# Kernel optimization log

Measured on AMD Instinct MI355X. Metric: run time of the kernel, lower is better.

The kernel has to match this reference:

```python
import jax, jax.numpy as jnp
import numpy as np

DIM, HEAD, R = 192, 8, 3
RR = 2 * R + 1
RA = RR * RR  # 49-sample local window


def conv2d(x, w, b):
    y = jax.lax.conv_general_dilated(x, w, (1, 1), 'SAME',
                                     dimension_numbers=('NCHW', 'OIHW', 'NCHW'))
    return y + b[None, :, None, None]


def _pix(c, size):
    # normalized [-1,1] -> pixel coord, align_corners=False
    return (c + 1.0) * (size * 0.5) - 0.5


def _gather(img, iy, ix, valid=None):
    # img [B,C,H,W]; iy/ix int [B,...] -> [B,C,...]; zero-fill where not valid
    B, C, H, W = img.shape
    sh = iy.shape
    idx = (jnp.clip(iy, 0, H - 1) * W + jnp.clip(ix, 0, W - 1)).reshape(B, -1)
    g = jax.vmap(lambda f, i: f[:, i])(img.reshape(B, C, H * W), idx)
    g = g.reshape((B, C) + sh[1:])
    if valid is not None:
        g = g * valid.reshape((B, 1) + sh[1:]).astype(g.dtype)
    return g


def bilinear_sample(img, cy, cx, border=False):
    # F.grid_sample bilinear, align_corners=False; cy/cx [B,Q] -> [B,C,Q]
    B, C, H, W = img.shape
    py, px = _pix(cy, H), _pix(cx, W)
    y0f, x0f = jnp.floor(py), jnp.floor(px)
    wy, wx = py - y0f, px - x0f
    y0, x0 = y0f.astype(jnp.int32), x0f.astype(jnp.int32)
    out = 0.0
    for dy, sy in ((0, 1.0 - wy), (1, wy)):
        for dx, sx in ((0, 1.0 - wx), (1, wx)):
            iy, ix = y0 + dy, x0 + dx
            valid = None if border else ((iy >= 0) & (iy < H) & (ix >= 0) & (ix < W))
            out = out + _gather(img, iy, ix, valid) * (sy * sx)[:, None]
    return out


def nearest_sample(img, cy, cx):
    # F.grid_sample nearest, align_corners=False, padding_mode='zeros'
    B, C, H, W = img.shape
    iy = jnp.floor(_pix(cy, H) + 0.5).astype(jnp.int32)
    ix = jnp.floor(_pix(cx, W) + 0.5).astype(jnp.int32)
    valid = (iy >= 0) & (iy < H) & (ix >= 0) & (ix < W)
    return _gather(img, iy, ix, valid)


def mlp(x, ws, bs):
    for w, b in zip(ws[:-1], bs[:-1]):
        x = jax.nn.relu(x @ w + b)
    return x @ ws[-1] + bs[-1]


def reference(inp, sample_coord, cell, enc_w, enc_b, ch_w, ch_b, q_w, q_b,
              k_w, k_b, v_w, v_b, m0w, m0b, m1w, m1b, m2w, m2b, m3w, m3b, m4w, m4b):
    # gen_feat: encoder (conv stand-in) -> conv_ch -> q/k/v convs
    feat = conv2d(conv2d(inp, enc_w, enc_b), ch_w, ch_b)
    feat_q = conv2d(feat, q_w, q_b)
    feat_k = conv2d(feat, k_w, k_b)
    feat_v = conv2d(feat, v_w, v_b)
    B, _, H, W = feat.shape
    Q = sample_coord.shape[1]
    hd = DIM // HEAD

    cy, cx = sample_coord[..., 0], sample_coord[..., 1]
    # sample_coord_k: nearest LR pixel-center coords (grid_sample nearest over make_coord grid)
    iy = jnp.clip(jnp.floor(_pix(cy, H) + 0.5), 0, H - 1)
    ix = jnp.clip(jnp.floor(_pix(cx, W) + 0.5), 0, W - 1)
    sky = -1.0 + (2.0 * iy + 1.0) / H
    skx = -1.0 + (2.0 * ix + 1.0) / W

    dh = jnp.linspace(-R, R, RR, dtype=jnp.float32) * (2.0 / H)
    dw = jnp.linspace(-R, R, RR, dtype=jnp.float32) * (2.0 / W)
    gy, gx = jnp.meshgrid(dh, dw, indexing='ij')
    cky = sky[..., None] + gy.reshape(-1)  # [B,Q,RA]
    ckx = skx[..., None] + gx.reshape(-1)

    q = bilinear_sample(feat_q, cy, cx)                       # [B,DIM,Q]
    q = q.transpose(0, 2, 1).reshape(B, Q, HEAD, hd)
    k = nearest_sample(feat_k, cky, ckx)                      # [B,DIM,Q,RA]
    k = k.transpose(0, 2, 3, 1).reshape(B, Q, RA, HEAD, hd)
    v = nearest_sample(feat_v, cky, ckx)
    v = v.transpose(0, 2, 3, 1).reshape(B, Q, RA, HEAD, hd)

    attn = jnp.einsum('bqhd,bqrhd->bqrh', q, k) / np.sqrt(hd).astype(np.float32)
    attn = jax.nn.softmax(attn, axis=2)                       # softmax over window
    v = (v * attn[..., None]).reshape(B, Q, RA * DIM)         # weighted, NOT summed

    rel_cell = cell[:, None, :] * jnp.array([H, W], jnp.float32)
    rel_cell = jnp.broadcast_to(rel_cell, (B, Q, 2))
    feat_in = jnp.concatenate([v, rel_cell], axis=-1)         # [B,Q,DIM*RA+2]

    pred = mlp(feat_in, [m0w, m1w, m2w, m3w, m4w], [m0b, m1b, m2b, m3b, m4b])
    base = bilinear_sample(inp, cy, cx, border=True).transpose(0, 2, 1)  # [B,Q,3]
    return pred + base


def setup_inputs() -> dict:
    key = jax.random.key(0)
    ks = jax.random.split(key, 16)
    B, H, W, Q = 2, 64, 64, 4096
    enc_out, hidden = 64, 256
    in_dim = DIM * RA + 2

    def cw(k, o, i):
        return jax.random.normal(k, (o, i, 3, 3), jnp.float32) / np.sqrt(i * 9.0)

    def lw(k, i, o):
        return jax.random.normal(k, (i, o), jnp.float32) / np.sqrt(float(i))

    return {
        'inp': jax.random.normal(ks[0], (B, 3, H, W), jnp.float32),
        'sample_coord': jax.random.uniform(ks[1], (B, Q, 2), jnp.float32, -1.0, 1.0),
        'cell': jnp.full((B, 2), 2.0 / 128.0, jnp.float32),
        'enc_w': cw(ks[2], enc_out, 3), 'enc_b': jnp.zeros((enc_out,), jnp.float32),
        'ch_w': cw(ks[3], DIM, enc_out), 'ch_b': jnp.zeros((DIM,), jnp.float32),
        'q_w': cw(ks[4], DIM, DIM), 'q_b': jnp.zeros((DIM,), jnp.float32),
        'k_w': cw(ks[5], DIM, DIM), 'k_b': jnp.zeros((DIM,), jnp.float32),
        'v_w': cw(ks[6], DIM, DIM), 'v_b': jnp.zeros((DIM,), jnp.float32),
        'm0w': lw(ks[7], in_dim, hidden), 'm0b': jnp.zeros((hidden,), jnp.float32),
        'm1w': lw(ks[8], hidden, hidden), 'm1b': jnp.zeros((hidden,), jnp.float32),
        'm2w': lw(ks[9], hidden, hidden), 'm2b': jnp.zeros((hidden,), jnp.float32),
        'm3w': lw(ks[10], hidden, hidden), 'm3b': jnp.zeros((hidden,), jnp.float32),
        'm4w': lw(ks[11], hidden, 3), 'm4b': jnp.zeros((3,), jnp.float32),
    }
```

## Files before the change

kernel.cpp:

```cpp
#include <hip/hip_runtime.h>
#include <hip/hip_bf16.h>


constexpr int BB = 2, QQ = 4096, DIMC = 192, RAW = 49;
constexpr int ENC = 64, P1 = 66, P3 = 70;

typedef __attribute__((ext_vector_type(8))) short bf16x8;
typedef __attribute__((ext_vector_type(8))) unsigned short u16x8;
typedef __attribute__((ext_vector_type(4))) float f32x4;

__device__ inline short f2bf(float f) {
  __hip_bfloat16 h = __float2bfloat16(f);
  return __builtin_bit_cast(short, h);
}
__device__ inline float bf2f(unsigned short u) {
  return __uint_as_float(((unsigned)u) << 16);
}

constexpr long long N_F1 = (long long)BB * P1 * P1 * ENC;
constexpr long long N_FT = (long long)BB * P1 * P1 * DIMC;
constexpr long long N_FKS = (long long)BB * P3 * P3 * DIMC;
constexpr long long F_F1 = 0;
constexpr long long F_FEAT = F_F1 + N_F1;
constexpr long long F_FQ = F_FEAT + N_FT;
constexpr long long F_FKB = F_FQ + N_FT;
constexpr long long F_FVB = F_FKB + N_FKS / 2;
constexpr long long F_ZEND = F_FVB + N_FKS / 2;
constexpr long long F_ATTN = F_ZEND;
constexpr long long F_HA = F_ATTN + (long long)BB * QQ * RAW * 8;
constexpr long long F_HB = F_HA + 8192LL * 256;
constexpr long long F_W0T = F_HB + 8192LL * 256;
constexpr long long F_WTCHB = F_W0T + (256LL * 9408) / 2;
constexpr long long F_WTQB = F_WTCHB + (192LL * 576) / 2;
constexpr long long F_WTKB = F_WTQB + (192LL * 1728) / 2;
constexpr long long F_WTVB = F_WTKB + (192LL * 1728) / 2;
constexpr long long ZERO_N4 = F_ZEND / 4;

__global__ __launch_bounds__(256) void k_zero(float4* p, int n4) {
  int i = blockIdx.x * 256 + threadIdx.x;
  float4 z = make_float4(0.f, 0.f, 0.f, 0.f);
  for (; i < n4; i += gridDim.x * 256) p[i] = z;
}

__global__ __launch_bounds__(256) void k_w0t(const float* __restrict__ w0,
                                             short* __restrict__ w0t) {
  __shared__ short sh[64][72];
  int k0 = blockIdx.x * 64, n0 = blockIdx.y * 64;
  int t = threadIdx.x;
  #pragma unroll
  for (int i = 0; i < 16; i++) {
    int idx = t + i * 256;
    int r = idx >> 6, cc = idx & 63;
    sh[cc][r] = f2bf(w0[(long long)(k0 + r) * 256 + n0 + cc]);
  }
  __syncthreads();
  #pragma unroll
  for (int i = 0; i < 16; i++) {
    int idx = t + i * 256;
    int n = idx >> 6, k = idx & 63;
    w0t[(long long)(n0 + n) * 9408 + k0 + k] = sh[n][k];
  }
}

__global__ __launch_bounds__(256) void k_wtb(const float* __restrict__ w,
                                             short* __restrict__ wtb, int CI, int CO) {
  int g = blockIdx.x * 256 + threadIdx.x;
  if (g >= CO * CI * 9) return;
  int co = g / (CI * 9);
  int r = g - co * CI * 9;
  int ci = r / 9, t = r - ci * 9;
  wtb[(long long)co * (9 * CI) + t * CI + ci] = f2bf(w[g]);
}

__global__ __launch_bounds__(256) void k_conv1(const float* __restrict__ inp,
                                               const float* __restrict__ ew,
                                               const float* __restrict__ eb,
                                               float* __restrict__ f1p) {
  int g = blockIdx.x * 256 + threadIdx.x;
  int co = g & 63, x = (g >> 6) & 63, y = (g >> 12) & 63, b = g >> 18;
  float acc = eb[co];
  #pragma unroll
  for (int ci = 0; ci < 3; ci++)
    #pragma unroll
    for (int ky = 0; ky < 3; ky++) {
      int yy = y + ky - 1;
      if (yy < 0 || yy > 63) continue;
      #pragma unroll
      for (int kx = 0; kx < 3; kx++) {
        int xx = x + kx - 1;
        if (xx < 0 || xx > 63) continue;
        acc += inp[((b * 3 + ci) * 64 + yy) * 64 + xx] * ew[((co * 3 + ci) * 3 + ky) * 3 + kx];
      }
    }
  f1p[((b * P1 + y + 1) * P1 + (x + 1)) * ENC + co] = acc;
}

template <int CIN, bool OB16>
__global__ __launch_bounds__(256) void k_conv3x3m(const float* __restrict__ in,
                                                  const short* __restrict__ wtb,
                                                  const float* __restrict__ bias,
                                                  void* __restrict__ outv, int pitchO,
                                                  int padO, int COUT) {
  constexpr int NCH = CIN / 64;
  int nb = blockIdx.x;
  int by = blockIdx.y;
  int b = by >> 6, y = by & 63;
  int t = threadIdx.x;
  int lane = t & 63, w = t >> 6, wr = w >> 1, wc = w & 1;
  __shared__ __align__(16) short As[64][72];
  __shared__ __align__(16) short Bs[64][72];
  f32x4 acc[2][2];
  #pragma unroll
  for (int i = 0; i < 2; i++)
    #pragma unroll
    for (int j = 0; j < 2; j++) acc[i][j] = (f32x4){0.f, 0.f, 0.f, 0.f};
  int arow = t >> 2, kq = t & 3;
  int nbase = nb * 64;
  const long long K9 = 9LL * CIN;
  for (int c = 0; c < 9 * NCH; c++) {
    int t9 = c / NCH, sub = c - t9 * NCH;
    int dy = t9 / 3 - 1, dx = t9 % 3 - 1;
    __syncthreads();
    {
      const float* src = in + (((long long)b * P1 + y + dy + 1) * P1 + (arow + dx + 1)) * CIN +
                         sub * 64 + kq * 16;
      bf16x8 pk0, pk1;
      #pragma unroll
      for (int j = 0; j < 2; j++) {
        float4 v = *(const float4*)(src + j * 4);
        pk0[j * 4 + 0] = f2bf(v.x);
        pk0[j * 4 + 1] = f2bf(v.y);
        pk0[j * 4 + 2] = f2bf(v.z);
        pk0[j * 4 + 3] = f2bf(v.w);
      }
      #pragma unroll
      for (int j = 0; j < 2; j++) {
        float4 v = *(const float4*)(src + 8 + j * 4);
        pk1[j * 4 + 0] = f2bf(v.x);
        pk1[j * 4 + 1] = f2bf(v.y);
        pk1[j * 4 + 2] = f2bf(v.z);
        pk1[j * 4 + 3] = f2bf(v.w);
      }
      *(bf16x8*)&As[arow][kq * 16] = pk0;
      *(bf16x8*)&As[arow][kq * 16 + 8] = pk1;
      const short* wp = wtb + (long long)(nbase + arow) * K9 + c * 64 + kq * 16;
      *(bf16x8*)&Bs[arow][kq * 16] = *(const bf16x8*)wp;
      *(bf16x8*)&Bs[arow][kq * 16 + 8] = *(const bf16x8*)(wp + 8);
    }
    __syncthreads();
    #pragma unroll
    for (int kk = 0; kk < 2; kk++) {
      bf16x8 a0 = *(const bf16x8*)&As[wr * 32 + (lane & 15)][kk * 32 + (lane >> 4) * 8];
      bf16x8 a1 = *(const bf16x8*)&As[wr * 32 + 16 + (lane & 15)][kk * 32 + (lane >> 4) * 8];
      bf16x8 b0 = *(const bf16x8*)&Bs[wc * 32 + (lane & 15)][kk * 32 + (lane >> 4) * 8];
      bf16x8 b1 = *(const bf16x8*)&Bs[wc * 32 + 16 + (lane & 15)][kk * 32 + (lane >> 4) * 8];
      acc[0][0] = __builtin_amdgcn_mfma_f32_16x16x32_bf16(a0, b0, acc[0][0], 0, 0, 0);
      acc[0][1] = __builtin_amdgcn_mfma_f32_16x16x32_bf16(a0, b1, acc[0][1], 0, 0, 0);
      acc[1][0] = __builtin_amdgcn_mfma_f32_16x16x32_bf16(a1, b0, acc[1][0], 0, 0, 0);
      acc[1][1] = __builtin_amdgcn_mfma_f32_16x16x32_bf16(a1, b1, acc[1][1], 0, 0, 0);
    }
  }
  int col0 = nbase + wc * 32 + (lane & 15);
  int row0 = wr * 32 + ((lane >> 4) << 2);
  #pragma unroll
  for (int nf = 0; nf < 2; nf++) {
    int co = col0 + nf * 16;
    float bv = bias[co];
    #pragma unroll
    for (int mf = 0; mf < 2; mf++)
      #pragma unroll
      for (int i = 0; i < 4; i++) {
        int x = row0 + mf * 16 + i;
        long long oi = (((long long)b * pitchO + y + padO) * pitchO + (x + padO)) * COUT + co;
        float val = acc[mf][nf][i] + bv;
        if (OB16) ((short*)outv)[oi] = f2bf(val);
        else ((float*)outv)[oi] = val;
      }
  }
}

__global__ __launch_bounds__(64) void k_attn(const float* __restrict__ sc,
                                             const float* __restrict__ fq,
                                             const unsigned short* __restrict__ fkb,
                                             float* __restrict__ attnO) {
  int bq = blockIdx.x;
  int b = bq >> 12;
  int lane = threadIdx.x;
  float cy = sc[bq * 2 + 0], cx = sc[bq * 2 + 1];
  float py = (cy + 1.f) * 32.f - 0.5f, px = (cx + 1.f) * 32.f - 0.5f;
  float fy = floorf(py), fx = floorf(px);
  float wy = py - fy, wx = px - fx;
  int iy = (int)fy, ix = (int)fx;
  __shared__ __align__(16) float qv[192];
  {
    const float* base = fq + (((long long)b * P1 + iy + 1) * P1 + (ix + 1)) * DIMC;
    #pragma unroll
    for (int u = 0; u < 3; u++) {
      int c = lane * 3 + u;
      float v00 = base[c], v01 = base[DIMC + c];
      float v10 = base[P1 * DIMC + c], v11 = base[P1 * DIMC + DIMC + c];
      qv[c] = (1.f - wy) * ((1.f - wx) * v00 + wx * v01) +
              wy * ((1.f - wx) * v10 + wx * v11);
    }
  }
  __syncthreads();
  int icy = min(max((int)floorf(py + 0.5f), 0), 63);
  int icx = min(max((int)floorf(px + 0.5f), 0), 63);
  float l[8];
  #pragma unroll
  for (int h = 0; h < 8; h++) l[h] = -1e30f;
  if (lane < 49) {
    int dy = lane / 7 - 3, dx = lane % 7 - 3;
    const unsigned short* kb =
        fkb + (((long long)b * P3 + icy + dy + 3) * P3 + (icx + dx + 3)) * DIMC;
    #pragma unroll
    for (int h = 0; h < 8; h++) l[h] = 0.f;
    #pragma unroll
    for (int c8 = 0; c8 < 24; c8++) {
      u16x8 k8 = *(const u16x8*)(kb + c8 * 8);
      float4 qa = *(const float4*)&qv[c8 * 8];
      float4 qb = *(const float4*)&qv[c8 * 8 + 4];
      l[c8 / 3] += qa.x * bf2f(k8[0]) + qa.y * bf2f(k8[1]) + qa.z * bf2f(k8[2]) +
                   qa.w * bf2f(k8[3]) + qb.x * bf2f(k8[4]) + qb.y * bf2f(k8[5]) +
                   qb.z * bf2f(k8[6]) + qb.w * bf2f(k8[7]);
    }
    const float s = 0.20412414523193154f;
    #pragma unroll
    for (int h = 0; h < 8; h++) l[h] *= s;
  }
  float a[8];
  #pragma unroll
  for (int h = 0; h < 8; h++) {
    float mx = l[h];
    #pragma unroll
    for (int s = 1; s < 64; s <<= 1) mx = fmaxf(mx, __shfl_xor(mx, s));
    float e = (lane < 49) ? expf(l[h] - mx) : 0.f;
    float sm = e;
    #pragma unroll
    for (int s = 1; s < 64; s <<= 1) sm += __shfl_xor(sm, s);
    a[h] = e / sm;
  }
  if (lane < 49) {
    float* op = attnO + ((long long)bq * 49 + lane) * 8;
    *(float4*)op = make_float4(a[0], a[1], a[2], a[3]);
    *(float4*)(op + 4) = make_float4(a[4], a[5], a[6], a[7]);
  }
}

__global__ __launch_bounds__(256) void k_l0m(const float* __restrict__ sc,
                                             const float* __restrict__ cell,
                                             const unsigned short* __restrict__ fvb,
                                             const float* __restrict__ attn,
                                             const short* __restrict__ w0t,
                                             const float* __restrict__ w0,
                                             const float* __restrict__ b0,
                                             float* __restrict__ hout) {
  int lin = blockIdx.y * 4 + blockIdx.x;
  int swz = (lin & 7) * 64 + (lin >> 3);
  int nb = swz & 3, mb = swz >> 2;
  int qbase = mb * 64;
  int b = qbase >> 12;
  int t = threadIdx.x;
  int lane = t & 63, w = t >> 6, wr = w >> 1, wc = w & 1;
  __shared__ __align__(16) short As[64][72];
  __shared__ __align__(16) short Bs[64][72];
  int arow = t >> 2, kq = t & 3;
  int q = qbase + arow;
  float cy = sc[q * 2 + 0], cx = sc[q * 2 + 1];
  float py = (cy + 1.f) * 32.f - 0.5f, px = (cx + 1.f) * 32.f - 0.5f;
  int icy = min(max((int)floorf(py + 0.5f), 0), 63);
  int icx = min(max((int)floorf(px + 0.5f), 0), 63);
  const unsigned short* fvp = fvb + (((long long)b * P3 + icy + 3) * P3 + (icx + 3)) * DIMC;
  const float* ap = attn + (long long)q * 49 * 8;
  f32x4 acc[2][2];
  #pragma unroll
  for (int i = 0; i < 2; i++)
    #pragma unroll
    for (int j = 0; j < 2; j++) acc[i][j] = (f32x4){0.f, 0.f, 0.f, 0.f};
  int nbase = nb * 64;
  for (int c = 0; c < 147; c++) {
    int r = c / 3, sub = c - r * 3;
    int dy2 = r / 7 - 3, dx2 = r % 7 - 3;
    long long tap = ((long long)dy2 * P3 + dx2) * DIMC;
    __syncthreads();
    {
      const unsigned short* src = fvp + tap + sub * 64 + kq * 16;
      u16x8 r0 = *(const u16x8*)src;
      u16x8 r1 = *(const u16x8*)(src + 8);
      bf16x8 pk0, pk1;
      #pragma unroll
      for (int j = 0; j < 2; j++) {
        float a = ap[r * 8 + (sub * 64 + kq * 16 + j * 4) / 24];
        #pragma unroll
        for (int e = 0; e < 4; e++) pk0[j * 4 + e] = f2bf(bf2f(r0[j * 4 + e]) * a);
      }
      #pragma unroll
      for (int j = 2; j < 4; j++) {
        float a = ap[r * 8 + (sub * 64 + kq * 16 + j * 4) / 24];
        #pragma unroll
        for (int e = 0; e < 4; e++) pk1[(j - 2) * 4 + e] = f2bf(bf2f(r1[(j - 2) * 4 + e]) * a);
      }
      *(bf16x8*)&As[arow][kq * 16] = pk0;
      *(bf16x8*)&As[arow][kq * 16 + 8] = pk1;
      const short* wp = w0t + (long long)(nbase + arow) * 9408 + c * 64 + kq * 16;
      *(bf16x8*)&Bs[arow][kq * 16] = *(const bf16x8*)wp;
      *(bf16x8*)&Bs[arow][kq * 16 + 8] = *(const bf16x8*)(wp + 8);
    }
    __syncthreads();
    #pragma unroll
    for (int kk = 0; kk < 2; kk++) {
      bf16x8 a0 = *(const bf16x8*)&As[wr * 32 + (lane & 15)][kk * 32 + (lane >> 4) * 8];
      bf16x8 a1 = *(const bf16x8*)&As[wr * 32 + 16 + (lane & 15)][kk * 32 + (lane >> 4) * 8];
      bf16x8 b0 = *(const bf16x8*)&Bs[wc * 32 + (lane & 15)][kk * 32 + (lane >> 4) * 8];
      bf16x8 b1 = *(const bf16x8*)&Bs[wc * 32 + 16 + (lane & 15)][kk * 32 + (lane >> 4) * 8];
      acc[0][0] = __builtin_amdgcn_mfma_f32_16x16x32_bf16(a0, b0, acc[0][0], 0, 0, 0);
      acc[0][1] = __builtin_amdgcn_mfma_f32_16x16x32_bf16(a0, b1, acc[0][1], 0, 0, 0);
      acc[1][0] = __builtin_amdgcn_mfma_f32_16x16x32_bf16(a1, b0, acc[1][0], 0, 0, 0);
      acc[1][1] = __builtin_amdgcn_mfma_f32_16x16x32_bf16(a1, b1, acc[1][1], 0, 0, 0);
    }
  }
  float rc0 = cell[b * 2 + 0] * 64.f, rc1 = cell[b * 2 + 1] * 64.f;
  int col0 = nbase + wc * 32 + (lane & 15);
  int row0 = wr * 32 + ((lane >> 4) << 2);
  #pragma unroll
  for (int nf = 0; nf < 2; nf++) {
    int n = col0 + nf * 16;
    float tailv = rc0 * w0[9408LL * 256 + n] + rc1 * w0[9409LL * 256 + n] + b0[n];
    #pragma unroll
    for (int mf = 0; mf < 2; mf++)
      #pragma unroll
      for (int i = 0; i < 4; i++)
        hout[(long long)(qbase + row0 + mf * 16 + i) * 256 + n] =
            fmaxf(acc[mf][nf][i] + tailv, 0.f);
  }
}

template <bool RELU>
__global__ __launch_bounds__(256) void k_fc(const float* __restrict__ hin,
                                            const float* __restrict__ w,
                                            const float* __restrict__ bias,
                                            float* __restrict__ hout) {
  int nb = blockIdx.x, mb = blockIdx.y;
  int qbase = mb * 64, nbase = nb * 64;
  int tid = threadIdx.x;
  int tx = tid & 15, ty = tid >> 4;
  __shared__ __align__(16) float As[16][64];
  __shared__ __align__(16) float Ws[16][64];
  float acc[4][4] = {};
  int ms = tid >> 2, js = tid & 3;
  int kw = tid >> 4, n4 = tid & 15;
  for (int kc = 0; kc < 16; kc++) {
    __syncthreads();
    float4 av = *(const float4*)(hin + ((long long)(qbase + ms)) * 256 + kc * 16 + js * 4);
    As[js * 4 + 0][ms] = av.x;
    As[js * 4 + 1][ms] = av.y;
    As[js * 4 + 2][ms] = av.z;
    As[js * 4 + 3][ms] = av.w;
    *(float4*)&Ws[kw][n4 * 4] =
        *(const float4*)(w + ((long long)(kc * 16 + kw)) * 256 + nbase + n4 * 4);
    __syncthreads();
    #pragma unroll
    for (int k = 0; k < 16; k++) {
      float4 a4 = *(const float4*)&As[k][ty * 4];
      float4 b4 = *(const float4*)&Ws[k][tx * 4];
      float aa[4] = {a4.x, a4.y, a4.z, a4.w};
      float bb[4] = {b4.x, b4.y, b4.z, b4.w};
      #pragma unroll
      for (int i = 0; i < 4; i++)
        #pragma unroll
        for (int j = 0; j < 4; j++) acc[i][j] += aa[i] * bb[j];
    }
  }
  #pragma unroll
  for (int i = 0; i < 4; i++) {
    float4 o;
    #pragma unroll
    for (int j = 0; j < 4; j++) {
      float v = acc[i][j] + bias[nbase + tx * 4 + j];
      if (RELU) v = fmaxf(v, 0.f);
      ((float*)&o)[j] = v;
    }
    *(float4*)(hout + ((long long)(qbase + ty * 4 + i)) * 256 + nbase + tx * 4) = o;
  }
}

__global__ __launch_bounds__(64) void k_final(const float* __restrict__ h3,
                                              const float* __restrict__ w4,
                                              const float* __restrict__ b4,
                                              const float* __restrict__ sc,
                                              const float* __restrict__ inp,
                                              float* __restrict__ out) {
  int bq = blockIdx.x;
  int b = bq >> 12;
  int lane = threadIdx.x;
  float p0 = 0.f, p1 = 0.f, p2 = 0.f;
  const float* hr = h3 + (long long)bq * 256;
  #pragma unroll
  for (int u = 0; u < 4; u++) {
    int c = lane + u * 64;
    float hv = hr[c];
    p0 += hv * w4[c * 3 + 0];
    p1 += hv * w4[c * 3 + 1];
    p2 += hv * w4[c * 3 + 2];
  }
  #pragma unroll
  for (int s = 1; s < 64; s <<= 1) {
    p0 += __shfl_xor(p0, s);
    p1 += __shfl_xor(p1, s);
    p2 += __shfl_xor(p2, s);
  }
  if (lane == 0) {
    float cy = sc[bq * 2 + 0], cx = sc[bq * 2 + 1];
    float py = (cy + 1.f) * 32.f - 0.5f, px = (cx + 1.f) * 32.f - 0.5f;
    float fy = floorf(py), fx = floorf(px);
    float wy = py - fy, wx = px - fx;
    int y0 = (int)fy, x0 = (int)fx;
    int yc0 = min(max(y0, 0), 63), yc1 = min(max(y0 + 1, 0), 63);
    int xc0 = min(max(x0, 0), 63), xc1 = min(max(x0 + 1, 0), 63);
    float o[3] = {p0 + b4[0], p1 + b4[1], p2 + b4[2]};
    #pragma unroll
    for (int j = 0; j < 3; j++) {
      const float* im = inp + ((long long)b * 3 + j) * 4096;
      float s00 = im[yc0 * 64 + xc0], s01 = im[yc0 * 64 + xc1];
      float s10 = im[yc1 * 64 + xc0], s11 = im[yc1 * 64 + xc1];
      o[j] += (1.f - wy) * ((1.f - wx) * s00 + wx * s01) +
              wy * ((1.f - wx) * s10 + wx * s11);
      out[(long long)bq * 3 + j] = o[j];
    }
  }
}

extern "C" void kernel_launch(void* const* d_in, const int* in_sizes, int n_in,
                              void* d_out, int out_size, void* d_ws, size_t ws_size,
                              hipStream_t stream) {
  const float* inp = (const float*)d_in[0];
  const float* sc = (const float*)d_in[1];
  const float* cell = (const float*)d_in[2];
  const float* enc_w = (const float*)d_in[3];
  const float* enc_b = (const float*)d_in[4];
  const float* ch_w = (const float*)d_in[5];
  const float* ch_b = (const float*)d_in[6];
  const float* q_w = (const float*)d_in[7];
  const float* q_b = (const float*)d_in[8];
  const float* k_w = (const float*)d_in[9];
  const float* k_b = (const float*)d_in[10];
  const float* v_w = (const float*)d_in[11];
  const float* v_b = (const float*)d_in[12];
  const float* m0w = (const float*)d_in[13];
  const float* m0b = (const float*)d_in[14];
  const float* m1w = (const float*)d_in[15];
  const float* m1b = (const float*)d_in[16];
  const float* m2w = (const float*)d_in[17];
  const float* m2b = (const float*)d_in[18];
  const float* m3w = (const float*)d_in[19];
  const float* m3b = (const float*)d_in[20];
  const float* m4w = (const float*)d_in[21];
  const float* m4b = (const float*)d_in[22];
  float* ws = (float*)d_ws;
  float* f1p = ws + F_F1;
  float* featp = ws + F_FEAT;
  float* featqp = ws + F_FQ;
  unsigned short* fkb = (unsigned short*)(ws + F_FKB);
  unsigned short* fvb = (unsigned short*)(ws + F_FVB);
  float* attnb = ws + F_ATTN;
  float* h_a = ws + F_HA;
  float* h_b = ws + F_HB;
  short* w0t = (short*)(ws + F_W0T);
  short* wtb_ch = (short*)(ws + F_WTCHB);
  short* wtb_q = (short*)(ws + F_WTQB);
  short* wtb_k = (short*)(ws + F_WTKB);
  short* wtb_v = (short*)(ws + F_WTVB);
  float* outp = (float*)d_out;

  k_zero<<<2048, 256, 0, stream>>>((float4*)ws, (int)ZERO_N4);
  k_w0t<<<dim3(147, 4), 256, 0, stream>>>(m0w, w0t);
  k_wtb<<<(192 * 64 * 9 + 255) / 256, 256, 0, stream>>>(ch_w, wtb_ch, 64, 192);
  k_wtb<<<(192 * 192 * 9 + 255) / 256, 256, 0, stream>>>(q_w, wtb_q, 192, 192);
  k_wtb<<<(192 * 192 * 9 + 255) / 256, 256, 0, stream>>>(k_w, wtb_k, 192, 192);
  k_wtb<<<(192 * 192 * 9 + 255) / 256, 256, 0, stream>>>(v_w, wtb_v, 192, 192);
  k_conv1<<<(BB * 64 * 64 * ENC) / 256, 256, 0, stream>>>(inp, enc_w, enc_b, f1p);
  k_conv3x3m<64, false><<<dim3(3, BB * 64), 256, 0, stream>>>(f1p, wtb_ch, ch_b, featp, P1, 1, DIMC);
  k_conv3x3m<192, false><<<dim3(3, BB * 64), 256, 0, stream>>>(featp, wtb_q, q_b, featqp, P1, 1, DIMC);
  k_conv3x3m<192, true><<<dim3(3, BB * 64), 256, 0, stream>>>(featp, wtb_k, k_b, fkb, P3, 3, DIMC);
  k_conv3x3m<192, true><<<dim3(3, BB * 64), 256, 0, stream>>>(featp, wtb_v, v_b, fvb, P3, 3, DIMC);
  k_attn<<<BB * QQ, 64, 0, stream>>>(sc, featqp, fkb, attnb);
  k_l0m<<<dim3(4, 128), 256, 0, stream>>>(sc, cell, fvb, attnb, w0t, m0w, m0b, h_a);
  k_fc<true><<<dim3(4, 128), 256, 0, stream>>>(h_a, m1w, m1b, h_b);
  k_fc<true><<<dim3(4, 128), 256, 0, stream>>>(h_b, m2w, m2b, h_a);
  k_fc<true><<<dim3(4, 128), 256, 0, stream>>>(h_a, m3w, m3b, h_b);
  k_final<<<BB * QQ, 64, 0, stream>>>(h_b, m4w, m4b, sc, inp, outp);
}
```

Measured before the change: 480.6 us.

## Store intermediates in bf16, split-K first MLP layer, MFMA for hidden FC layers

Conv intermediates (f1, feat), attention weights and MLP hidden activations are now stored as bf16 instead of fp32, which halves memory traffic and removes per-tile conversion inside the conv loader. The first MLP layer is restructured into a two-way split-K GEMM with 64x128 tiles, writing fp32 partials that a new reduction kernel sums, adds the cell/bias tail and applies ReLU. The three hidden FC layers switch from an fp32 scalar-FMA GEMM to bf16 MFMA using pre-transposed weights. The trade is extra launches, a partial-sum round trip through memory, and lower precision in the activations.

```diff
diff --git a/kernel.cpp b/kernel.cpp
--- a/kernel.cpp
+++ b/kernel.cpp
@@ -17,24 +17,24 @@
   return __uint_as_float(((unsigned)u) << 16);
 }
 
-constexpr long long N_F1 = (long long)BB * P1 * P1 * ENC;
-constexpr long long N_FT = (long long)BB * P1 * P1 * DIMC;
-constexpr long long N_FKS = (long long)BB * P3 * P3 * DIMC;
 constexpr long long F_F1 = 0;
-constexpr long long F_FEAT = F_F1 + N_F1;
-constexpr long long F_FQ = F_FEAT + N_FT;
-constexpr long long F_FKB = F_FQ + N_FT;
-constexpr long long F_FVB = F_FKB + N_FKS / 2;
-constexpr long long F_ZEND = F_FVB + N_FKS / 2;
-constexpr long long F_ATTN = F_ZEND;
-constexpr long long F_HA = F_ATTN + (long long)BB * QQ * RAW * 8;
-constexpr long long F_HB = F_HA + 8192LL * 256;
-constexpr long long F_W0T = F_HB + 8192LL * 256;
-constexpr long long F_WTCHB = F_W0T + (256LL * 9408) / 2;
-constexpr long long F_WTQB = F_WTCHB + (192LL * 576) / 2;
-constexpr long long F_WTKB = F_WTQB + (192LL * 1728) / 2;
-constexpr long long F_WTVB = F_WTKB + (192LL * 1728) / 2;
-constexpr long long ZERO_N4 = F_ZEND / 4;
+constexpr long long F_FEAT = 278784;
+constexpr long long F_FQ = 1115136;
+constexpr long long ZA_END = 2787840;
+constexpr long long F_PART = 0;
+constexpr long long F_FKB = 4194304;
+constexpr long long F_FVB = 5135104;
+constexpr long long F_ATTN = 6075904;
+constexpr long long F_W0T = 7681536;
+constexpr long long F_WTCH = 8885760;
+constexpr long long F_WTQ = 8941056;
+constexpr long long F_WTK = 9106944;
+constexpr long long F_WTV = 9272832;
+constexpr long long F_WFC1 = 9438720;
+constexpr long long F_WFC2 = 9471488;
+constexpr long long F_WFC3 = 9504256;
+constexpr long long F_HA = 9537024;
+constexpr long long F_HB = 10585600;
 
 __global__ __launch_bounds__(256) void k_zero(float4* p, int n4) {
   int i = blockIdx.x * 256 + threadIdx.x;
@@ -72,10 +72,16 @@
   wtb[(long long)co * (9 * CI) + t * CI + ci] = f2bf(w[g]);
 }
 
+__global__ __launch_bounds__(256) void k_wfc(const float* __restrict__ w,
+                                             short* __restrict__ wt) {
+  int n = blockIdx.x, k = threadIdx.x;
+  wt[n * 256 + k] = f2bf(w[k * 256 + n]);
+}
+
 __global__ __launch_bounds__(256) void k_conv1(const float* __restrict__ inp,
                                                const float* __restrict__ ew,
                                                const float* __restrict__ eb,
-                                               float* __restrict__ f1p) {
+                                               unsigned short* __restrict__ f1p) {
   int g = blockIdx.x * 256 + threadIdx.x;
   int co = g & 63, x = (g >> 6) & 63, y = (g >> 12) & 63, b = g >> 18;
   float acc = eb[co];
@@ -92,15 +98,15 @@
         acc += inp[((b * 3 + ci) * 64 + yy) * 64 + xx] * ew[((co * 3 + ci) * 3 + ky) * 3 + kx];
       }
     }
-  f1p[((b * P1 + y + 1) * P1 + (x + 1)) * ENC + co] = acc;
-}
-
-template <int CIN, bool OB16>
-__global__ __launch_bounds__(256) void k_conv3x3m(const float* __restrict__ in,
+  f1p[((b * P1 + y + 1) * P1 + (x + 1)) * ENC + co] = (unsigned short)f2bf(acc);
+}
+
+template <int CIN, bool OF32>
+__global__ __launch_bounds__(256) void k_conv3x3m(const unsigned short* __restrict__ in,
                                                   const short* __restrict__ wtb,
                                                   const float* __restrict__ bias,
                                                   void* __restrict__ outv, int pitchO,
-                                                  int padO, int COUT) {
+                                                  int padO) {
   constexpr int NCH = CIN / 64;
   int nb = blockIdx.x;
   int by = blockIdx.y;
@@ -114,7 +120,7 @@
   for (int i = 0; i < 2; i++)
     #pragma unroll
     for (int j = 0; j < 2; j++) acc[i][j] = (f32x4){0.f, 0.f, 0.f, 0.f};
-  int arow = t >> 2, kq = t & 3;
+  int arow = t >> 2, kq4 = t & 3;
   int nbase = nb * 64;
   const long long K9 = 9LL * CIN;
   for (int c = 0; c < 9 * NCH; c++) {
@@ -122,30 +128,13 @@
     int dy = t9 / 3 - 1, dx = t9 % 3 - 1;
     __syncthreads();
     {
-      const float* src = in + (((long long)b * P1 + y + dy + 1) * P1 + (arow + dx + 1)) * CIN +
-                         sub * 64 + kq * 16;
-      bf16x8 pk0, pk1;
-      #pragma unroll
-      for (int j = 0; j < 2; j++) {
-        float4 v = *(const float4*)(src + j * 4);
-        pk0[j * 4 + 0] = f2bf(v.x);
-        pk0[j * 4 + 1] = f2bf(v.y);
-        pk0[j * 4 + 2] = f2bf(v.z);
-        pk0[j * 4 + 3] = f2bf(v.w);
-      }
-      #pragma unroll
-      for (int j = 0; j < 2; j++) {
-        float4 v = *(const float4*)(src + 8 + j * 4);
-        pk1[j * 4 + 0] = f2bf(v.x);
-        pk1[j * 4 + 1] = f2bf(v.y);
-        pk1[j * 4 + 2] = f2bf(v.z);
-        pk1[j * 4 + 3] = f2bf(v.w);
-      }
-      *(bf16x8*)&As[arow][kq * 16] = pk0;
-      *(bf16x8*)&As[arow][kq * 16 + 8] = pk1;
-      const short* wp = wtb + (long long)(nbase + arow) * K9 + c * 64 + kq * 16;
-      *(bf16x8*)&Bs[arow][kq * 16] = *(const bf16x8*)wp;
-      *(bf16x8*)&Bs[arow][kq * 16 + 8] = *(const bf16x8*)(wp + 8);
+      const unsigned short* src = in +
+          (((long long)b * P1 + y + dy + 1) * P1 + (arow + dx + 1)) * CIN + sub * 64 + kq4 * 16;
+      *(bf16x8*)&As[arow][kq4 * 16] = *(const bf16x8*)src;
+      *(bf16x8*)&As[arow][kq4 * 16 + 8] = *(const bf16x8*)(src + 8);
+      const short* wp = wtb + (long long)(nbase + arow) * K9 + c * 64 + kq4 * 16;
+      *(bf16x8*)&Bs[arow][kq4 * 16] = *(const bf16x8*)wp;
+      *(bf16x8*)&Bs[arow][kq4 * 16 + 8] = *(const bf16x8*)(wp + 8);
     }
     __syncthreads();
     #pragma unroll
@@ -171,10 +160,10 @@
       #pragma unroll
       for (int i = 0; i < 4; i++) {
         int x = row0 + mf * 16 + i;
-        long long oi = (((long long)b * pitchO + y + padO) * pitchO + (x + padO)) * COUT + co;
+        long long oi = (((long long)b * pitchO + y + padO) * pitchO + (x + padO)) * DIMC + co;
         float val = acc[mf][nf][i] + bv;
-        if (OB16) ((short*)outv)[oi] = f2bf(val);
-        else ((float*)outv)[oi] = val;
+        if (OF32) ((float*)outv)[oi] = val;
+        else ((unsigned short*)outv)[oi] = (unsigned short)f2bf(val);
       }
   }
 }
@@ -182,7 +171,7 @@
 __global__ __launch_bounds__(64) void k_attn(const float* __restrict__ sc,
                                              const float* __restrict__ fq,
                                              const unsigned short* __restrict__ fkb,
-                                             float* __restrict__ attnO) {
+                                             unsigned short* __restrict__ attnO) {
   int bq = blockIdx.x;
   int b = bq >> 12;
   int lane = threadIdx.x;
@@ -228,7 +217,7 @@
     #pragma unroll
     for (int h = 0; h < 8; h++) l[h] *= s;
   }
-  float a[8];
+  bf16x8 a8;
   #pragma unroll
   for (int h = 0; h < 8; h++) {
     float mx = l[h];
@@ -238,153 +227,175 @@
     float sm = e;
     #pragma unroll
     for (int s = 1; s < 64; s <<= 1) sm += __shfl_xor(sm, s);
-    a[h] = e / sm;
+    a8[h] = f2bf(e / sm);
   }
   if (lane < 49) {
-    float* op = attnO + ((long long)bq * 49 + lane) * 8;
-    *(float4*)op = make_float4(a[0], a[1], a[2], a[3]);
-    *(float4*)(op + 4) = make_float4(a[4], a[5], a[6], a[7]);
+    *(bf16x8*)(attnO + ((long long)bq * 49 + lane) * 8) = a8;
   }
 }
 
 __global__ __launch_bounds__(256) void k_l0m(const float* __restrict__ sc,
-                                             const float* __restrict__ cell,
                                              const unsigned short* __restrict__ fvb,
-                                             const float* __restrict__ attn,
+                                             const unsigned short* __restrict__ attn,
                                              const short* __restrict__ w0t,
-                                             const float* __restrict__ w0,
-                                             const float* __restrict__ b0,
-                                             float* __restrict__ hout) {
-  int lin = blockIdx.y * 4 + blockIdx.x;
-  int swz = (lin & 7) * 64 + (lin >> 3);
-  int nb = swz & 3, mb = swz >> 2;
+                                             float* __restrict__ part) {
+  int L = blockIdx.x + (blockIdx.y << 2);
+  int xcd = L & 7, slot = L >> 3;
+  int kq = xcd >> 2, nh = (xcd >> 1) & 1;
+  int mb = ((xcd & 1) << 6) | slot;
   int qbase = mb * 64;
-  int b = qbase >> 12;
+  int b = mb >> 6;
   int t = threadIdx.x;
   int lane = t & 63, w = t >> 6, wr = w >> 1, wc = w & 1;
   __shared__ __align__(16) short As[64][72];
-  __shared__ __align__(16) short Bs[64][72];
-  int arow = t >> 2, kq = t & 3;
+  __shared__ __align__(16) short Bs[128][72];
+  int arow = t >> 2, kq4 = t & 3;
   int q = qbase + arow;
   float cy = sc[q * 2 + 0], cx = sc[q * 2 + 1];
   float py = (cy + 1.f) * 32.f - 0.5f, px = (cx + 1.f) * 32.f - 0.5f;
   int icy = min(max((int)floorf(py + 0.5f), 0), 63);
   int icx = min(max((int)floorf(px + 0.5f), 0), 63);
   const unsigned short* fvp = fvb + (((long long)b * P3 + icy + 3) * P3 + (icx + 3)) * DIMC;
-  const float* ap = attn + (long long)q * 49 * 8;
-  f32x4 acc[2][2];
+  const unsigned short* ap = attn + (long long)q * 392;
+  int ch0 = kq4 * 16;
+  int nbase = nh * 128;
+  int nB = t >> 1, hB = t & 1;
+  f32x4 acc[2][4];
   #pragma unroll
   for (int i = 0; i < 2; i++)
     #pragma unroll
-    for (int j = 0; j < 2; j++) acc[i][j] = (f32x4){0.f, 0.f, 0.f, 0.f};
-  int nbase = nb * 64;
-  for (int c = 0; c < 147; c++) {
-    int r = c / 3, sub = c - r * 3;
+    for (int j = 0; j < 4; j++) acc[i][j] = (f32x4){0.f, 0.f, 0.f, 0.f};
+  int c0 = kq * 74, cnt = kq ? 73 : 74;
+  for (int ci = 0; ci < cnt; ci++) {
+    int cc = c0 + ci;
+    int r = cc / 3, sub = cc - r * 3;
     int dy2 = r / 7 - 3, dx2 = r % 7 - 3;
     long long tap = ((long long)dy2 * P3 + dx2) * DIMC;
     __syncthreads();
     {
-      const unsigned short* src = fvp + tap + sub * 64 + kq * 16;
+      const unsigned short* src = fvp + tap + sub * 64 + ch0;
       u16x8 r0 = *(const u16x8*)src;
       u16x8 r1 = *(const u16x8*)(src + 8);
+      int cA = sub * 64 + ch0;
+      float a0 = bf2f(ap[r * 8 + cA / 24]);
+      float a1 = bf2f(ap[r * 8 + (cA + 8) / 24]);
       bf16x8 pk0, pk1;
       #pragma unroll
-      for (int j = 0; j < 2; j++) {
-        float a = ap[r * 8 + (sub * 64 + kq * 16 + j * 4) / 24];
+      for (int e = 0; e < 8; e++) pk0[e] = f2bf(bf2f(r0[e]) * a0);
+      #pragma unroll
+      for (int e = 0; e < 8; e++) pk1[e] = f2bf(bf2f(r1[e]) * a1);
+      *(bf16x8*)&As[arow][ch0] = pk0;
+      *(bf16x8*)&As[arow][ch0 + 8] = pk1;
+      const short* wp = w0t + (long long)(nbase + nB) * 9408 + cc * 64 + hB * 32;
+      *(bf16x8*)&Bs[nB][hB * 32] = *(const bf16x8*)wp;
+      *(bf16x8*)&Bs[nB][hB * 32 + 8] = *(const bf16x8*)(wp + 8);
+      *(bf16x8*)&Bs[nB][hB * 32 + 16] = *(const bf16x8*)(wp + 16);
+      *(bf16x8*)&Bs[nB][hB * 32 + 24] = *(const bf16x8*)(wp + 24);
+    }
+    __syncthreads();
+    #pragma unroll
+    for (int kk = 0; kk < 2; kk++) {
+      bf16x8 av[2], bv[4];
+      #pragma unroll
+      for (int mf = 0; mf < 2; mf++)
+        av[mf] = *(const bf16x8*)&As[wr * 32 + mf * 16 + (lane & 15)][kk * 32 + (lane >> 4) * 8];
+      #pragma unroll
+      for (int nf = 0; nf < 4; nf++)
+        bv[nf] = *(const bf16x8*)&Bs[wc * 64 + nf * 16 + (lane & 15)][kk * 32 + (lane >> 4) * 8];
+      #pragma unroll
+      for (int mf = 0; mf < 2; mf++)
         #pragma unroll
-        for (int e = 0; e < 4; e++) pk0[j * 4 + e] = f2bf(bf2f(r0[j * 4 + e]) * a);
-      }
-      #pragma unroll
-      for (int j = 2; j < 4; j++) {
-        float a = ap[r * 8 + (sub * 64 + kq * 16 + j * 4) / 24];
-        #pragma unroll
-        for (int e = 0; e < 4; e++) pk1[(j - 2) * 4 + e] = f2bf(bf2f(r1[(j - 2) * 4 + e]) * a);
-      }
-      *(bf16x8*)&As[arow][kq * 16] = pk0;
-      *(bf16x8*)&As[arow][kq * 16 + 8] = pk1;
-      const short* wp = w0t + (long long)(nbase + arow) * 9408 + c * 64 + kq * 16;
-      *(bf16x8*)&Bs[arow][kq * 16] = *(const bf16x8*)wp;
-      *(bf16x8*)&Bs[arow][kq * 16 + 8] = *(const bf16x8*)(wp + 8);
-    }
-    __syncthreads();
-    #pragma unroll
-    for (int kk = 0; kk < 2; kk++) {
-      bf16x8 a0 = *(const bf16x8*)&As[wr * 32 + (lane & 15)][kk * 32 + (lane >> 4) * 8];
-      bf16x8 a1 = *(const bf16x8*)&As[wr * 32 + 16 + (lane & 15)][kk * 32 + (lane >> 4) * 8];
-      bf16x8 b0 = *(const bf16x8*)&Bs[wc * 32 + (lane & 15)][kk * 32 + (lane >> 4) * 8];
-      bf16x8 b1 = *(const bf16x8*)&Bs[wc * 32 + 16 + (lane & 15)][kk * 32 + (lane >> 4) * 8];
-      acc[0][0] = __builtin_amdgcn_mfma_f32_16x16x32_bf16(a0, b0, acc[0][0], 0, 0, 0);
-      acc[0][1] = __builtin_amdgcn_mfma_f32_16x16x32_bf16(a0, b1, acc[0][1], 0, 0, 0);
-      acc[1][0] = __builtin_amdgcn_mfma_f32_16x16x32_bf16(a1, b0, acc[1][0], 0, 0, 0);
-      acc[1][1] = __builtin_amdgcn_mfma_f32_16x16x32_bf16(a1, b1, acc[1][1], 0, 0, 0);
-    }
-  }
+        for (int nf = 0; nf < 4; nf++)
+          acc[mf][nf] = __builtin_amdgcn_mfma_f32_16x16x32_bf16(av[mf], bv[nf], acc[mf][nf], 0, 0, 0);
+    }
+  }
+  float* p = part + (long long)kq * 2097152;
+  int row0 = wr * 32 + ((lane >> 4) << 2);
+  int col0 = nbase + wc * 64 + (lane & 15);
+  #pragma unroll
+  for (int mf = 0; mf < 2; mf++)
+    #pragma unroll
+    for (int nf = 0; nf < 4; nf++)
+      #pragma unroll
+      for (int i = 0; i < 4; i++)
+        p[(long long)(qbase + row0 + mf * 16 + i) * 256 + col0 + nf * 16] = acc[mf][nf][i];
+}
+
+__global__ __launch_bounds__(256) void k_l0red(const float* __restrict__ part,
+                                               const float* __restrict__ cell,
+                                               const float* __restrict__ w0,
+                                               const float* __restrict__ b0,
+                                               unsigned short* __restrict__ h) {
+  int gid = blockIdx.x * 256 + threadIdx.x;
+  int q = gid >> 6, n0 = (gid & 63) << 2;
+  int b = q >> 12;
   float rc0 = cell[b * 2 + 0] * 64.f, rc1 = cell[b * 2 + 1] * 64.f;
+  float4 s0 = ((const float4*)part)[gid];
+  float4 s1 = ((const float4*)(part + 2097152))[gid];
+  unsigned short o[4];
+  #pragma unroll
+  for (int j = 0; j < 4; j++) {
+    int n = n0 + j;
+    float tailv = rc0 * w0[9408LL * 256 + n] + rc1 * w0[9409LL * 256 + n] + b0[n];
+    float v = ((const float*)&s0)[j] + ((const float*)&s1)[j] + tailv;
+    o[j] = (unsigned short)f2bf(fmaxf(v, 0.f));
+  }
+  *(uint2*)(h + (long long)gid * 4) = *(uint2*)o;
+}
+
+__global__ __launch_bounds__(256) void k_fcm(const unsigned short* __restrict__ hin,
+                                             const short* __restrict__ wt,
+                                             const float* __restrict__ bias,
+                                             unsigned short* __restrict__ hout) {
+  int nb = blockIdx.x, mb = blockIdx.y;
+  int qbase = mb * 64, nbase = nb * 64;
+  int t = threadIdx.x;
+  int lane = t & 63, w = t >> 6, wr = w >> 1, wc = w & 1;
+  __shared__ __align__(16) short As[64][264];
+  __shared__ __align__(16) short Bs[64][264];
+  int row = t >> 2, seg = t & 3;
+  {
+    const unsigned short* hp = hin + (long long)(qbase + row) * 256 + seg * 64;
+    const short* wp = wt + (long long)(nbase + row) * 256 + seg * 64;
+    #pragma unroll
+    for (int j = 0; j < 8; j++) {
+      *(bf16x8*)&As[row][seg * 64 + j * 8] = *(const bf16x8*)(hp + j * 8);
+      *(bf16x8*)&Bs[row][seg * 64 + j * 8] = *(const bf16x8*)(wp + j * 8);
+    }
+  }
+  __syncthreads();
+  f32x4 acc[2][2];
+  #pragma unroll
+  for (int i = 0; i < 2; i++)
+    #pragma unroll
+    for (int j = 0; j < 2; j++) acc[i][j] = (f32x4){0.f, 0.f, 0.f, 0.f};
+  #pragma unroll
+  for (int kk = 0; kk < 8; kk++) {
+    bf16x8 a0 = *(const bf16x8*)&As[wr * 32 + (lane & 15)][kk * 32 + (lane >> 4) * 8];
+    bf16x8 a1 = *(const bf16x8*)&As[wr * 32 + 16 + (lane & 15)][kk * 32 + (lane >> 4) * 8];
+    bf16x8 b0 = *(const bf16x8*)&Bs[wc * 32 + (lane & 15)][kk * 32 + (lane >> 4) * 8];
+    bf16x8 b1 = *(const bf16x8*)&Bs[wc * 32 + 16 + (lane & 15)][kk * 32 + (lane >> 4) * 8];
+    acc[0][0] = __builtin_amdgcn_mfma_f32_16x16x32_bf16(a0, b0, acc[0][0], 0, 0, 0);
+    acc[0][1] = __builtin_amdgcn_mfma_f32_16x16x32_bf16(a0, b1, acc[0][1], 0, 0, 0);
+    acc[1][0] = __builtin_amdgcn_mfma_f32_16x16x32_bf16(a1, b0, acc[1][0], 0, 0, 0);
+    acc[1][1] = __builtin_amdgcn_mfma_f32_16x16x32_bf16(a1, b1, acc[1][1], 0, 0, 0);
+  }
+  int row0 = wr * 32 + ((lane >> 4) << 2);
   int col0 = nbase + wc * 32 + (lane & 15);
-  int row0 = wr * 32 + ((lane >> 4) << 2);
   #pragma unroll
   for (int nf = 0; nf < 2; nf++) {
     int n = col0 + nf * 16;
-    float tailv = rc0 * w0[9408LL * 256 + n] + rc1 * w0[9409LL * 256 + n] + b0[n];
+    float bv = bias[n];
     #pragma unroll
     for (int mf = 0; mf < 2; mf++)
       #pragma unroll
       for (int i = 0; i < 4; i++)
         hout[(long long)(qbase + row0 + mf * 16 + i) * 256 + n] =
-            fmaxf(acc[mf][nf][i] + tailv, 0.f);
-  }
-}
-
-template <bool RELU>
-__global__ __launch_bounds__(256) void k_fc(const float* __restrict__ hin,
-                                            const float* __restrict__ w,
-                                            const float* __restrict__ bias,
-                                            float* __restrict__ hout) {
-  int nb = blockIdx.x, mb = blockIdx.y;
-  int qbase = mb * 64, nbase = nb * 64;
-  int tid = threadIdx.x;
-  int tx = tid & 15, ty = tid >> 4;
-  __shared__ __align__(16) float As[16][64];
-  __shared__ __align__(16) float Ws[16][64];
-  float acc[4][4] = {};
-  int ms = tid >> 2, js = tid & 3;
-  int kw = tid >> 4, n4 = tid & 15;
-  for (int kc = 0; kc < 16; kc++) {
-    __syncthreads();
-    float4 av = *(const float4*)(hin + ((long long)(qbase + ms)) * 256 + kc * 16 + js * 4);
-    As[js * 4 + 0][ms] = av.x;
-    As[js * 4 + 1][ms] = av.y;
-    As[js * 4 + 2][ms] = av.z;
-    As[js * 4 + 3][ms] = av.w;
-    *(float4*)&Ws[kw][n4 * 4] =
-        *(const float4*)(w + ((long long)(kc * 16 + kw)) * 256 + nbase + n4 * 4);
-    __syncthreads();
-    #pragma unroll
-    for (int k = 0; k < 16; k++) {
-      float4 a4 = *(const float4*)&As[k][ty * 4];
-      float4 b4 = *(const float4*)&Ws[k][tx * 4];
-      float aa[4] = {a4.x, a4.y, a4.z, a4.w};
-      float bb[4] = {b4.x, b4.y, b4.z, b4.w};
-      #pragma unroll
-      for (int i = 0; i < 4; i++)
-        #pragma unroll
-        for (int j = 0; j < 4; j++) acc[i][j] += aa[i] * bb[j];
-    }
-  }
-  #pragma unroll
-  for (int i = 0; i < 4; i++) {
-    float4 o;
-    #pragma unroll
-    for (int j = 0; j < 4; j++) {
-      float v = acc[i][j] + bias[nbase + tx * 4 + j];
-      if (RELU) v = fmaxf(v, 0.f);
-      ((float*)&o)[j] = v;
-    }
-    *(float4*)(hout + ((long long)(qbase + ty * 4 + i)) * 256 + nbase + tx * 4) = o;
-  }
-}
-
-__global__ __launch_bounds__(64) void k_final(const float* __restrict__ h3,
+            (unsigned short)f2bf(fmaxf(acc[mf][nf][i] + bv, 0.f));
+  }
+}
+
+__global__ __launch_bounds__(64) void k_final(const unsigned short* __restrict__ h3,
                                               const float* __restrict__ w4,
                                               const float* __restrict__ b4,
                                               const float* __restrict__ sc,
@@ -394,11 +405,11 @@
   int b = bq >> 12;
   int lane = threadIdx.x;
   float p0 = 0.f, p1 = 0.f, p2 = 0.f;
-  const float* hr = h3 + (long long)bq * 256;
+  const unsigned short* hr = h3 + (long long)bq * 256;
   #pragma unroll
   for (int u = 0; u < 4; u++) {
     int c = lane + u * 64;
-    float hv = hr[c];
+    float hv = bf2f(hr[c]);
     p0 += hv * w4[c * 3 + 0];
     p1 += hv * w4[c * 3 + 1];
     p2 += hv * w4[c * 3 + 2];
@@ -457,36 +468,45 @@
   const float* m4w = (const float*)d_in[21];
   const float* m4b = (const float*)d_in[22];
   float* ws = (float*)d_ws;
-  float* f1p = ws + F_F1;
-  float* featp = ws + F_FEAT;
+  unsigned short* f1p = (unsigned short*)(ws + F_F1);
+  unsigned short* featp = (unsigned short*)(ws + F_FEAT);
   float* featqp = ws + F_FQ;
+  float* part = ws + F_PART;
   unsigned short* fkb = (unsigned short*)(ws + F_FKB);
   unsigned short* fvb = (unsigned short*)(ws + F_FVB);
-  float* attnb = ws + F_ATTN;
-  float* h_a = ws + F_HA;
-  float* h_b = ws + F_HB;
+  unsigned short* attnb = (unsigned short*)(ws + F_ATTN);
   short* w0t = (short*)(ws + F_W0T);
-  short* wtb_ch = (short*)(ws + F_WTCHB);
-  short* wtb_q = (short*)(ws + F_WTQB);
-  short* wtb_k = (short*)(ws + F_WTKB);
-  short* wtb_v = (short*)(ws + F_WTVB);
+  short* wtb_ch = (short*)(ws + F_WTCH);
+  short* wtb_q = (short*)(ws + F_WTQ);
+  short* wtb_k = (short*)(ws + F_WTK);
+  short* wtb_v = (short*)(ws + F_WTV);
+  short* wfc1 = (short*)(ws + F_WFC1);
+  short* wfc2 = (short*)(ws + F_WFC2);
+  short* wfc3 = (short*)(ws + F_WFC3);
+  unsigned short* h_a = (unsigned short*)(ws + F_HA);
+  unsigned short* h_b = (unsigned short*)(ws + F_HB);
   float* outp = (float*)d_out;
 
-  k_zero<<<2048, 256, 0, stream>>>((float4*)ws, (int)ZERO_N4);
+  k_zero<<<1024, 256, 0, stream>>>((float4*)ws, (int)(ZA_END / 4));
+  k_zero<<<1024, 256, 0, stream>>>((float4*)(ws + F_FKB), (int)(1881600 / 4));
   k_w0t<<<dim3(147, 4), 256, 0, stream>>>(m0w, w0t);
   k_wtb<<<(192 * 64 * 9 + 255) / 256, 256, 0, stream>>>(ch_w, wtb_ch, 64, 192);
   k_wtb<<<(192 * 192 * 9 + 255) / 256, 256, 0, stream>>>(q_w, wtb_q, 192, 192);
   k_wtb<<<(192 * 192 * 9 + 255) / 256, 256, 0, stream>>>(k_w, wtb_k, 192, 192);
   k_wtb<<<(192 * 192 * 9 + 255) / 256, 256, 0, stream>>>(v_w, wtb_v, 192, 192);
+  k_wfc<<<256, 256, 0, stream>>>(m1w, wfc1);
+  k_wfc<<<256, 256, 0, stream>>>(m2w, wfc2);
+  k_wfc<<<256, 256, 0, stream>>>(m3w, wfc3);
   k_conv1<<<(BB * 64 * 64 * ENC) / 256, 256, 0, stream>>>(inp, enc_w, enc_b, f1p);
-  k_conv3x3m<64, false><<<dim3(3, BB * 64), 256, 0, stream>>>(f1p, wtb_ch, ch_b, featp, P1, 1, DIMC);
-  k_conv3x3m<192, false><<<dim3(3, BB * 64), 256, 0, stream>>>(featp, wtb_q, q_b, featqp, P1, 1, DIMC);
-  k_conv3x3m<192, true><<<dim3(3, BB * 64), 256, 0, stream>>>(featp, wtb_k, k_b, fkb, P3, 3, DIMC);
-  k_conv3x3m<192, true><<<dim3(3, BB * 64), 256, 0, stream>>>(featp, wtb_v, v_b, fvb, P3, 3, DIMC);
+  k_conv3x3m<64, false><<<dim3(3, BB * 64), 256, 0, stream>>>(f1p, wtb_ch, ch_b, featp, P1, 1);
+  k_conv3x3m<192, true><<<dim3(3, BB * 64), 256, 0, stream>>>(featp, wtb_q, q_b, featqp, P1, 1);
+  k_conv3x3m<192, false><<<dim3(3, BB * 64), 256, 0, stream>>>(featp, wtb_k, k_b, fkb, P3, 3);
+  k_conv3x3m<192, false><<<dim3(3, BB * 64), 256, 0, stream>>>(featp, wtb_v, v_b, fvb, P3, 3);
   k_attn<<<BB * QQ, 64, 0, stream>>>(sc, featqp, fkb, attnb);
-  k_l0m<<<dim3(4, 128), 256, 0, stream>>>(sc, cell, fvb, attnb, w0t, m0w, m0b, h_a);
-  k_fc<true><<<dim3(4, 128), 256, 0, stream>>>(h_a, m1w, m1b, h_b);
-  k_fc<true><<<dim3(4, 128), 256, 0, stream>>>(h_b, m2w, m2b, h_a);
-  k_fc<true><<<dim3(4, 128), 256, 0, stream>>>(h_a, m3w, m3b, h_b);
+  k_l0m<<<dim3(4, 128), 256, 0, stream>>>(sc, fvb, attnb, w0t, part);
+  k_l0red<<<2048, 256, 0, stream>>>(part, cell, m0w, m0b, h_a);
+  k_fcm<<<dim3(4, 128), 256, 0, stream>>>(h_a, wfc1, m1b, h_b);
+  k_fcm<<<dim3(4, 128), 256, 0, stream>>>(h_b, wfc2, m2b, h_a);
+  k_fcm<<<dim3(4, 128), 256, 0, stream>>>(h_a, wfc3, m3b, h_b);
   k_final<<<BB * QQ, 64, 0, stream>>>(h_b, m4w, m4b, sc, inp, outp);
 }
```

After: 386.1 us. -19.7%, faster.
